# Kernel tuning notes

Hardware: AMD Instinct MI355X
Metric: run time of the kernel (lower is better)

Reference implementation:

```python
import jax, jax.numpy as jnp
import numpy as np

V, E, H, C = 100000, 300, 512, 3
SP, SH, B = 64, 32, 128


def lstm_scan(x, Wih, Whh, b):
    # x: [T, B, E]; PyTorch gate order i, f, g, o
    T, Bb, _ = x.shape
    Hh = Whh.shape[1]
    h0 = jnp.zeros((Bb, Hh), x.dtype)

    def step(carry, xt):
        h, c = carry
        g = xt @ Wih.T + h @ Whh.T + b
        i, f, gg, o = jnp.split(g, 4, axis=-1)
        c = jax.nn.sigmoid(f) * c + jax.nn.sigmoid(i) * jnp.tanh(gg)
        h = jax.nn.sigmoid(o) * jnp.tanh(c)
        return (h, c), h

    _, hs = jax.lax.scan(step, (h0, h0), x)
    return hs  # [T, B, H]


def setup_inputs() -> dict:
    key = jax.random.key(0)
    ks = jax.random.split(key, 20)
    inv_sqrt_h = 1.0 / np.sqrt(H).astype(np.float32)

    def u(k, shape, scale):
        return (jax.random.uniform(k, shape, jnp.float32) * 2.0 - 1.0) * scale

    embed_table = jax.random.normal(ks[4], (V, E), jnp.float32) * 0.1
    embed_table = embed_table.at[0].set(0.0)  # padding_idx=0
    return {
        "premise": jax.random.randint(ks[0], (SP, B), 1, V),
        "premise_len": jax.random.randint(ks[1], (B,), 1, SP + 1),
        "hypothesis": jax.random.randint(ks[2], (SH, B), 1, V),
        "hypothesis_len": jax.random.randint(ks[3], (B,), 1, SH + 1),
        "embed_table": embed_table,
        "p_Wih": u(ks[5], (4 * H, E), inv_sqrt_h),
        "p_Whh": u(ks[6], (4 * H, H), inv_sqrt_h),
        "p_b": u(ks[7], (4 * H,), inv_sqrt_h),
        "h_Wih": u(ks[8], (4 * H, E), inv_sqrt_h),
        "h_Whh": u(ks[9], (4 * H, H), inv_sqrt_h),
        "h_b": u(ks[10], (4 * H,), inv_sqrt_h),
        "m_Wih": u(ks[11], (4 * H, 2 * H), inv_sqrt_h),
        "m_Whh": u(ks[12], (4 * H, H), inv_sqrt_h),
        "m_b": u(ks[13], (4 * H,), inv_sqrt_h),
        "w_e": jax.random.uniform(ks[14], (H,), jnp.float32),
        "Ws": u(ks[15], (H, H), np.sqrt(6.0 / (2 * H)).astype(np.float32)),
        "Wt": u(ks[16], (H, H), np.sqrt(6.0 / (2 * H)).astype(np.float32)),
        "Wm": u(ks[17], (H, H), np.sqrt(6.0 / (2 * H)).astype(np.float32)),
        "fc_W": u(ks[18], (C, H), np.sqrt(6.0 / (H + C)).astype(np.float32)),
        "fc_b": jnp.zeros((C,), jnp.float32),
    }


def reference(premise, premise_len, hypothesis, hypothesis_len, embed_table,
              p_Wih, p_Whh, p_b, h_Wih, h_Whh, h_b, m_Wih, m_Whh, m_b,
              w_e, Ws, Wt, Wm, fc_W, fc_b):
    Sp, Bb = premise.shape
    Sh = hypothesis.shape[0]
    Hh = Ws.shape[0]

    # Encoder LSTMs; emulate pack/pad: outputs past length are zeros
    h_s = lstm_scan(embed_table[premise], p_Wih, p_Whh, p_b)  # [Sp,B,H]
    h_s = h_s * (jnp.arange(Sp)[:, None] < premise_len[None, :]).astype(h_s.dtype)[:, :, None]
    h_t = lstm_scan(embed_table[hypothesis], h_Wih, h_Whh, h_b)  # [Sh,B,H]
    h_t = h_t * (jnp.arange(Sh)[:, None] < hypothesis_len[None, :]).astype(h_t.dtype)[:, :, None]

    Ws_hs = jnp.einsum('sbe,he->sbh', h_s, Ws)  # precompute premise projection

    def step(carry, inputs):
        h_m, c_m, h_last = carry
        h_t_k, k = inputs
        q = h_t_k @ Wt.T + h_m @ Wm.T                              # [B,H]
        e = jnp.einsum('sbh,h->sb', jnp.tanh(Ws_hs + q[None]), w_e)  # [Sp,B]
        alpha = jax.nn.softmax(e, axis=0)                           # softmax over premise (no mask, as in original)
        a_k = jnp.einsum('sb,sbh->bh', alpha, h_s)
        m_k = jnp.concatenate([a_k, h_t_k], axis=1)                 # [B,2H]
        g = m_k @ m_Wih.T + h_m @ m_Whh.T + m_b
        i, f, gg, o = jnp.split(g, 4, axis=-1)
        c_new = jax.nn.sigmoid(f) * c_m + jax.nn.sigmoid(i) * jnp.tanh(gg)
        h_new = jax.nn.sigmoid(o) * jnp.tanh(c_new)
        h_last = jnp.where((k + 1 == hypothesis_len)[:, None], h_new, h_last)
        return (h_new, c_new, h_last), None

    z = jnp.zeros((Bb, Hh), h_s.dtype)
    (_, _, h_last), _ = jax.lax.scan(step, (z, z, z), (h_t, jnp.arange(Sh)))
    return h_last @ fc_W.T + fc_b  # [B, C]
```

## Files before the change

kernel.cpp:

```cpp
#include <hip/hip_runtime.h>


#define NWG 256
#define TPB 512

typedef float f8v __attribute__((ext_vector_type(8)));

#define O_XPP      0ull
#define O_HTMW     0ull
#define O_HTWT     8388608ull
#define O_WSHS     10485760ull
#define O_XPH      16777216ull
#define O_HST      25165824ull
#define O_HS2      29360128ull
#define O_HTT      33554432ull
#define O_WIHTP    35651584ull
#define O_WIHTH    36265984ull
#define O_WHHPP    36880384ull
#define O_WHHPH    37928960ull
#define O_DW       38977536ull
#define O_WST      41074688ull
#define O_WTT      41336832ull
#define O_MWIHRT   41598976ull
#define O_BPP      42647552ull
#define O_BPH      42649600ull
#define O_BPM      42651648ull
#define O_HT2      42653696ull
#define O_HMT2     42784768ull
#define O_QBUF     42915840ull
#define O_AK2      42981376ull
#define O_HLAST    43046912ull
#define WS_FLOATS  43112448ull

__device__ unsigned g_cnt = 0u;
__device__ unsigned g_gen = 0u;
__device__ unsigned g_arr[NWG * 16];
__device__ unsigned g_relA[16 * 16];
__device__ unsigned g_base = 0u;

struct Params {
  const int* premise; const int* plen; const int* hyp; const int* hlen;
  const float* embed;
  const float* pWih; const float* pWhh; const float* pb;
  const float* hWih; const float* hWhh; const float* hb;
  const float* mWih; const float* mWhh; const float* mb;
  const float* we; const float* Ws; const float* Wt; const float* Wm;
  const float* fcW; const float* fcb;
  float* out; float* ws;
};

__device__ __forceinline__ float2 sysld2(const float* p){
  unsigned long long u = __hip_atomic_load((const unsigned long long*)p,
      __ATOMIC_RELAXED, __HIP_MEMORY_SCOPE_SYSTEM);
  union { unsigned long long u; float2 f; } c; c.u = u; return c.f;
}
__device__ __forceinline__ void sysst(float* p, float v){
  union { float f; unsigned u; } c; c.f = v;
  __hip_atomic_store((unsigned*)p, c.u, __ATOMIC_RELAXED, __HIP_MEMORY_SCOPE_SYSTEM);
}

__device__ __forceinline__ void gbarH(){
  __syncthreads();
  if (threadIdx.x == 0){
    __threadfence();
    unsigned snap = __hip_atomic_load(&g_gen, __ATOMIC_RELAXED, __HIP_MEMORY_SCOPE_AGENT);
    unsigned n = __hip_atomic_fetch_add(&g_cnt, 1u, __ATOMIC_ACQ_REL, __HIP_MEMORY_SCOPE_AGENT);
    if ((n & 255u) == 255u){
      __hip_atomic_store(&g_gen, snap + 1u, __ATOMIC_RELEASE, __HIP_MEMORY_SCOPE_AGENT);
    } else {
      unsigned g;
      do {
        __builtin_amdgcn_s_sleep(2);
        g = __hip_atomic_load(&g_gen, __ATOMIC_ACQUIRE, __HIP_MEMORY_SCOPE_AGENT);
      } while ((int)(g - snap) <= 0);
    }
  }
  __syncthreads();
}

__device__ __forceinline__ void gbarL(unsigned e, int wg, int tid){
  __syncthreads();
  if (wg == 0){
    if (tid == 0)
      __hip_atomic_store(&g_arr[0], e, __ATOMIC_RELAXED, __HIP_MEMORY_SCOPE_SYSTEM);
    if (tid < NWG){
      while ((int)(__hip_atomic_load(&g_arr[tid*16], __ATOMIC_RELAXED,
                                     __HIP_MEMORY_SCOPE_SYSTEM) - e) < 0)
        __builtin_amdgcn_s_sleep(1);
    }
    __syncthreads();
    if (tid < 16)
      __hip_atomic_store(&g_relA[tid*16], e, __ATOMIC_RELAXED, __HIP_MEMORY_SCOPE_SYSTEM);
  } else {
    if (tid == 0){
      __hip_atomic_store(&g_arr[wg*16], e, __ATOMIC_RELAXED, __HIP_MEMORY_SCOPE_SYSTEM);
      while ((int)(__hip_atomic_load(&g_relA[(wg & 15)*16], __ATOMIC_RELAXED,
                                     __HIP_MEMORY_SCOPE_SYSTEM) - e) < 0)
        __builtin_amdgcn_s_sleep(1);
    }
    __syncthreads();
  }
}

__device__ __forceinline__ float sigf(float x){ return 1.0f/(1.0f + __expf(-x)); }
__device__ __forceinline__ float tanhf_(float x){ return 2.0f/(1.0f + __expf(-2.0f*x)) - 1.0f; }

__device__ __forceinline__ float wsum(float v){
  #pragma unroll
  for (int o = 32; o > 0; o >>= 1) v += __shfl_xor(v, o, 64);
  return v;
}
__device__ __forceinline__ float wmaxr(float v){
  #pragma unroll
  for (int o = 32; o > 0; o >>= 1) v = fmaxf(v, __shfl_xor(v, o, 64));
  return v;
}

__device__ void lstm_enc(int wg, int tid, int cg, int bg, int T,
    const float* __restrict__ XP, const float* __restrict__ WPair,
    const int* __restrict__ lens, float* hbuf,
    float* __restrict__ houtT, float* __restrict__ hout2, float* lds,
    unsigned& ep)
{
  const int b8 = tid & 7, hc32 = (tid >> 3) & 31, gp = tid >> 8;
  const int b = bg*8 + b8, hc = cg*32 + hc32;
  const float* wrow = WPair + (size_t)(hc*2 + gp) * 1024;
  const int mylen = lens[b];
  const int sb = tid >> 6, sk = (tid & 63) * 8;
  float* stage = lds;
  float* xch   = lds + 8*516;
  float c_reg = 0.f;

  for (int t = 0; t < T; ++t){
    const float* hin  = hbuf + (size_t)(t & 1) * 65536;
    float*       hout = hbuf + (size_t)((t + 1) & 1) * 65536;
    {
      const float* src = hin + (size_t)(bg*8 + sb)*512 + sk;
      float2 v0 = sysld2(src), v1 = sysld2(src+2), v2 = sysld2(src+4), v3 = sysld2(src+6);
      float* dst = stage + sb*516 + sk;
      float4 w0 = {v0.x, v0.y, v1.x, v1.y};
      float4 w1 = {v2.x, v2.y, v3.x, v3.y};
      *(float4*)dst = w0; *(float4*)(dst+4) = w1;
    }
    __syncthreads();
    float a0 = 0.f, a1 = 0.f;
    const float* hr = stage + b8*516;
    #pragma unroll 2
    for (int k = 0; k < 512; k += 4){
      float4 h4 = *(const float4*)(hr + k);
      float4 wA = *(const float4*)(wrow + k*2);
      float4 wB = *(const float4*)(wrow + k*2 + 4);
      a0 += h4.x*wA.x + h4.y*wA.z + h4.z*wB.x + h4.w*wB.z;
      a1 += h4.x*wA.y + h4.y*wA.w + h4.z*wB.y + h4.w*wB.w;
    }
    float2 xg = *(const float2*)(XP + ((size_t)t*128 + b)*2048 + hc*4 + gp*2);
    a0 += xg.x; a1 += xg.y;
    if (gp == 1){ xch[(b8*32+hc32)*2+0] = a0; xch[(b8*32+hc32)*2+1] = a1; }
    __syncthreads();
    if (gp == 0){
      float gg = xch[(b8*32+hc32)*2+0], go = xch[(b8*32+hc32)*2+1];
      float iv = sigf(a0), fv = sigf(a1), gv = tanhf_(gg), ov = sigf(go);
      c_reg = fv * c_reg + iv * gv;
      float hv = ov * tanhf_(c_reg);
      sysst(hout + (size_t)b*512 + hc, hv);
      float hm = (t < mylen) ? hv : 0.f;
      houtT[((size_t)t*512 + hc)*128 + b] = hm;
      if (hout2) hout2[((size_t)t*128 + b)*512 + hc] = hm;
    }
    ++ep; gbarL(ep, wg, tid);
  }
}

__global__ __launch_bounds__(TPB, 2) void mlstm(Params p){
  const int wg = blockIdx.x, tid = threadIdx.x;
  const int lane = tid & 63, wave = tid >> 6;
  const int gtid = wg * TPB + tid;
  const int gwave = wg * 8 + wave;
  const int cg = wg & 15, bg = wg >> 4;
  __shared__ float lds[8736];
  __shared__ unsigned sh_base;

  if (tid == 0)
    sh_base = __hip_atomic_load(&g_base, __ATOMIC_RELAXED, __HIP_MEMORY_SCOPE_SYSTEM);
  __syncthreads();
  unsigned ep = sh_base;

  float* const ws     = p.ws;
  float* const XPp    = ws + O_XPP;
  float* const XPh    = ws + O_XPH;
  float* const htmW   = ws + O_HTMW;
  float* const htWt   = ws + O_HTWT;
  float* const Ws_hs  = ws + O_WSHS;
  float* const h_sT   = ws + O_HST;
  float* const h_s2   = ws + O_HS2;
  float* const h_tT   = ws + O_HTT;
  float* const WihTp  = ws + O_WIHTP;
  float* const WihTh  = ws + O_WIHTH;
  float* const WhhPP  = ws + O_WHHPP;
  float* const WhhPH  = ws + O_WHHPH;
  float* const DW     = ws + O_DW;
  float* const WsT    = ws + O_WST;
  float* const WtT    = ws + O_WTT;
  float* const mWihRT = ws + O_MWIHRT;
  float* const bpP    = ws + O_BPP;
  float* const bpH    = ws + O_BPH;
  float* const bpM    = ws + O_BPM;
  float* const hT2    = ws + O_HT2;
  float* const hmT2   = ws + O_HMT2;
  float* const qbuf   = ws + O_QBUF;
  float* const ak2    = ws + O_AK2;
  float* const hlast  = ws + O_HLAST;

  for (int idx = gtid; idx < 300*2048; idx += NWG*TPB){
    int e = idx >> 11, jp = idx & 2047;
    int oc = (jp & 3) * 512 + (jp >> 2);
    WihTp[idx] = p.pWih[(size_t)oc*300 + e];
    WihTh[idx] = p.hWih[(size_t)oc*300 + e];
  }
  for (int idx = gtid; idx < 1024*512*2; idx += NWG*TPB){
    int g = idx & 1, k = (idx >> 1) & 511, pp = idx >> 10;
    int hc = pp >> 1, gp = pp & 1, oc = (gp*2+g)*512 + hc;
    WhhPP[idx] = p.pWhh[(size_t)oc*512 + k];
    WhhPH[idx] = p.hWhh[(size_t)oc*512 + k];
  }
  for (int idx = gtid; idx < 1024*1024*2; idx += NWG*TPB){
    int g = idx & 1, k = (idx >> 1) & 1023, pp = idx >> 11;
    int hc = pp >> 1, gp = pp & 1, oc = (gp*2+g)*512 + hc;
    DW[idx] = (k < 512) ? p.mWih[(size_t)oc*1024 + k]
                        : p.mWhh[(size_t)oc*512 + (k - 512)];
  }
  for (int idx = gtid; idx < 512*512; idx += NWG*TPB){
    int k = idx >> 9, h = idx & 511;
    WsT[idx] = p.Ws[(size_t)h*512 + k];
    WtT[idx] = p.Wt[(size_t)h*512 + k];
  }
  for (int idx = gtid; idx < 512*2048; idx += NWG*TPB){
    int k = idx >> 11, jp = idx & 2047;
    int oc = (jp & 3) * 512 + (jp >> 2);
    mWihRT[idx] = p.mWih[(size_t)oc*1024 + 512 + k];
  }
  for (int idx = gtid; idx < 2048; idx += NWG*TPB){
    int oc = (idx & 3) * 512 + (idx >> 2);
    bpP[idx] = p.pb[oc]; bpH[idx] = p.hb[oc]; bpM[idx] = p.mb[oc];
  }
  for (int idx = gtid; idx < 131072; idx += NWG*TPB){ hT2[idx] = 0.f; hmT2[idx] = 0.f; }
  gbarH();

  for (int task = gwave; task < 6144; task += NWG*8){
    const bool prem = task < 4096;
    int rb, cb;
    if (prem){ cb = task >> 10; rb = task & 1023; }
    else { int t2 = task - 4096; cb = t2 >> 9; rb = t2 & 511; }
    const int r0 = rb * 8;
    const int* toks = prem ? p.premise : p.hyp;
    const float* wT = prem ? WihTp : WihTh;
    const float* bias = prem ? bpP : bpH;
    float* outp = prem ? XPp : XPh;
    const int j0 = cb * 512 + lane * 8;
    const float* xr[8];
    #pragma unroll
    for (int r = 0; r < 8; ++r) xr[r] = p.embed + (size_t)toks[r0 + r] * 300;
    f8v bias8 = *(const f8v*)(bias + j0);
    float acc[8][8];
    #pragma unroll
    for (int r = 0; r < 8; ++r){
      #pragma unroll
      for (int i = 0; i < 8; ++i) acc[r][i] = 0.f;
    }
    for (int e = 0; e < 300; ++e){
      f8v w8 = *(const f8v*)(wT + (size_t)e * 2048 + j0);
      #pragma unroll
      for (int r = 0; r < 8; ++r){
        float xv = xr[r][e];
        #pragma unroll
        for (int i = 0; i < 8; ++i) acc[r][i] += xv * w8[i];
      }
    }
    #pragma unroll
    for (int r = 0; r < 8; ++r){
      f8v o8;
      #pragma unroll
      for (int i = 0; i < 8; ++i) o8[i] = acc[r][i] + bias8[i];
      *(f8v*)(outp + (size_t)(r0 + r) * 2048 + j0) = o8;
    }
  }
  gbarH();

  lstm_enc(wg, tid, cg, bg, 64, XPp, WhhPP, p.plen, hT2, h_sT, h_s2, lds, ep);
  for (int idx = gtid; idx < 65536; idx += NWG*TPB) sysst(hT2 + idx, 0.f);
  ++ep; gbarL(ep, wg, tid);
  lstm_enc(wg, tid, cg, bg, 32, XPh, WhhPH, p.hlen, hT2, h_tT, nullptr, lds, ep);
  gbarH();

  for (int task = gwave; task < 3584; task += NWG*8){
    const float* src; const float* wT; const float* bias; float* outp;
    int rb, cb, cols;
    if (task < 1024){ rb = task;        cb = 0;            src = h_sT; wT = WsT;    bias = nullptr; outp = Ws_hs; cols = 512; }
    else if (task < 1536){ rb = task-1024; cb = 0;         src = h_tT; wT = WtT;    bias = nullptr; outp = htWt;  cols = 512; }
    else { int t2 = task - 1536; cb = t2 >> 9; rb = t2 & 511; src = h_tT; wT = mWihRT; bias = bpM;  outp = htmW;  cols = 2048; }
    const int r0 = rb * 8;
    const int j0 = cb * 512 + lane * 8;
    const float* xr[8];
    #pragma unroll
    for (int r = 0; r < 8; ++r){
      int row = r0 + r;
      xr[r] = src + (size_t)(row >> 7) * 65536 + (row & 127);
    }
    f8v bias8 = {0,0,0,0,0,0,0,0};
    if (bias) bias8 = *(const f8v*)(bias + j0);
    float acc[8][8];
    #pragma unroll
    for (int r = 0; r < 8; ++r){
      #pragma unroll
      for (int i = 0; i < 8; ++i) acc[r][i] = 0.f;
    }
    for (int k = 0; k < 512; ++k){
      f8v w8 = *(const f8v*)(wT + (size_t)k * cols + j0);
      #pragma unroll
      for (int r = 0; r < 8; ++r){
        float xv = xr[r][(size_t)k * 128];
        #pragma unroll
        for (int i = 0; i < 8; ++i) acc[r][i] += xv * w8[i];
      }
    }
    #pragma unroll
    for (int r = 0; r < 8; ++r){
      f8v o8;
      #pragma unroll
      for (int i = 0; i < 8; ++i) o8[i] = acc[r][i] + bias8[i];
      *(f8v*)(outp + (size_t)(r0 + r) * (size_t)cols + j0) = o8;
    }
  }
  gbarH();

  const int b8 = tid & 7, hc32 = (tid >> 3) & 31, gp = tid >> 8;
  const int mb_ = bg*8 + b8, mhc = cg*32 + hc32;
  const float* dwrow = DW + (size_t)(mhc*2 + gp) * 2048;
  const int hyplen_b = p.hlen[mb_];
  const int sb = tid >> 6, sk = (tid & 63) * 8;
  float* stage  = lds;
  float* xchA   = lds + 8*516;
  float* stage2 = lds;
  float* xch2   = lds + 8*1028;
  float cm_reg = 0.f, hl_reg = 0.f;

  for (int k = 0; k < 32; ++k){
    const float* hmin  = hmT2 + (size_t)(k & 1) * 65536;
    float*       hmout = hmT2 + (size_t)((k + 1) & 1) * 65536;

    {
      {
        const float* src = hmin + (size_t)(bg*8 + sb)*512 + sk;
        float2 v0 = sysld2(src), v1 = sysld2(src+2), v2 = sysld2(src+4), v3 = sysld2(src+6);
        float* dst = stage + sb*516 + sk;
        float4 w0 = {v0.x, v0.y, v1.x, v1.y};
        float4 w1 = {v2.x, v2.y, v3.x, v3.y};
        *(float4*)dst = w0; *(float4*)(dst+4) = w1;
      }
      __syncthreads();
      const int c32 = (tid >> 3) & 31, half = tid >> 8;
      const int c = cg*32 + c32;
      float a = 0.f;
      const float* hr = stage + b8*516 + half*256;
      const float* wr = p.Wm + (size_t)c*512 + half*256;
      #pragma unroll 2
      for (int kk = 0; kk < 256; kk += 4){
        float4 h4 = *(const float4*)(hr + kk);
        float4 w4 = *(const float4*)(wr + kk);
        a += h4.x*w4.x + h4.y*w4.y + h4.z*w4.z + h4.w*w4.w;
      }
      if (half == 1) xchA[c32*8 + b8] = a;
      __syncthreads();
      if (half == 0){
        float v = a + xchA[c32*8 + b8] + htWt[((size_t)k*128 + mb_)*512 + c];
        sysst(qbuf + (size_t)mb_*512 + c, v);
      }
    }
    ++ep; gbarL(ep, wg, tid);

    if (wg < 128){
      const int bb = wg;
      const float* qb = qbuf + (size_t)bb*512 + lane*8;
      float2 qa = sysld2(qb), qbv = sysld2(qb+2), qc = sysld2(qb+4), qd = sysld2(qb+6);
      float4 q0 = {qa.x, qa.y, qbv.x, qbv.y};
      float4 q1 = {qc.x, qc.y, qd.x, qd.y};
      float4 e0 = *(const float4*)(p.we + lane*8);
      float4 e1 = *(const float4*)(p.we + lane*8 + 4);
      #pragma unroll
      for (int si = 0; si < 8; ++si){
        int s = wave*8 + si;
        const float* wsr = Ws_hs + ((size_t)s*128 + bb)*512 + lane*8;
        float4 s0 = *(const float4*)wsr;
        float4 s1 = *(const float4*)(wsr + 4);
        float v = tanhf_(s0.x + q0.x)*e0.x + tanhf_(s0.y + q0.y)*e0.y
                + tanhf_(s0.z + q0.z)*e0.z + tanhf_(s0.w + q0.w)*e0.w
                + tanhf_(s1.x + q1.x)*e1.x + tanhf_(s1.y + q1.y)*e1.y
                + tanhf_(s1.z + q1.z)*e1.z + tanhf_(s1.w + q1.w)*e1.w;
        v = wsum(v);
        if (lane == 0) lds[s] = v;
      }
      __syncthreads();
      if (wave == 0){
        float v = lds[lane];
        float m = wmaxr(v);
        float ex = __expf(v - m);
        float sm = wsum(ex);
        lds[64 + lane] = ex / sm;
      }
      __syncthreads();
      {
        float acc = 0.f;
        const float* hsb = h_s2 + (size_t)bb*512 + tid;
        #pragma unroll 4
        for (int s = 0; s < 64; s += 4){
          float4 al = *(const float4*)(lds + 64 + s);
          acc += al.x * hsb[(size_t)(s+0)*65536]
               + al.y * hsb[(size_t)(s+1)*65536]
               + al.z * hsb[(size_t)(s+2)*65536]
               + al.w * hsb[(size_t)(s+3)*65536];
        }
        sysst(ak2 + (size_t)bb*512 + tid, acc);
      }
    }
    ++ep; gbarL(ep, wg, tid);

    {
      {
        const int sb2 = tid >> 6, c0 = (tid & 63) * 16;
        const float* src = (c0 < 512) ? (ak2 + (size_t)(bg*8 + sb2)*512 + c0)
                                      : (hmin + (size_t)(bg*8 + sb2)*512 + (c0 - 512));
        float* dst = stage2 + sb2*1028 + c0;
        #pragma unroll
        for (int i = 0; i < 16; i += 4){
          float2 va = sysld2(src + i), vb = sysld2(src + i + 2);
          float4 w = {va.x, va.y, vb.x, vb.y};
          *(float4*)(dst + i) = w;
        }
      }
      __syncthreads();
      float a0 = 0.f, a1 = 0.f;
      const float* hr = stage2 + b8*1028;
      #pragma unroll 2
      for (int kk = 0; kk < 1024; kk += 4){
        float4 h4 = *(const float4*)(hr + kk);
        float4 wA = *(const float4*)(dwrow + kk*2);
        float4 wB = *(const float4*)(dwrow + kk*2 + 4);
        a0 += h4.x*wA.x + h4.y*wA.z + h4.z*wB.x + h4.w*wB.z;
        a1 += h4.x*wA.y + h4.y*wA.w + h4.z*wB.y + h4.w*wB.w;
      }
      float2 xg = *(const float2*)(htmW + ((size_t)k*128 + mb_)*2048 + mhc*4 + gp*2);
      a0 += xg.x; a1 += xg.y;
      if (gp == 1){ xch2[(b8*32+hc32)*2+0] = a0; xch2[(b8*32+hc32)*2+1] = a1; }
      __syncthreads();
      if (gp == 0){
        float gg = xch2[(b8*32+hc32)*2+0], go = xch2[(b8*32+hc32)*2+1];
        float iv = sigf(a0), fv = sigf(a1), gv = tanhf_(gg), ov = sigf(go);
        cm_reg = fv * cm_reg + iv * gv;
        float hv = ov * tanhf_(cm_reg);
        sysst(hmout + (size_t)mb_*512 + mhc, hv);
        if (k + 1 == hyplen_b) hl_reg = hv;
      }
    }
    ++ep; gbarL(ep, wg, tid);
  }

  if (gp == 0) hlast[(size_t)mb_*512 + mhc] = hl_reg;
  gbarH();

  if (wg == 0 && tid == 0)
    __hip_atomic_store(&g_base, ep, __ATOMIC_RELAXED, __HIP_MEMORY_SCOPE_SYSTEM);

  if (wg == 0){
    for (int o = wave; o < 384; o += 8){
      int bb = o / 3, cls = o - bb*3;
      const float* hr = hlast + (size_t)bb*512 + lane*8;
      const float* wr = p.fcW + (size_t)cls*512 + lane*8;
      float4 h0 = *(const float4*)hr, h1 = *(const float4*)(hr + 4);
      float4 w0 = *(const float4*)wr, w1 = *(const float4*)(wr + 4);
      float v = h0.x*w0.x + h0.y*w0.y + h0.z*w0.z + h0.w*w0.w
              + h1.x*w1.x + h1.y*w1.y + h1.z*w1.z + h1.w*w1.w;
      v = wsum(v);
      if (lane == 0) p.out[o] = v + p.fcb[cls];
    }
  }
}

extern "C" void kernel_launch(void* const* d_in, const int* in_sizes, int n_in,
                              void* d_out, int out_size, void* d_ws, size_t ws_size,
                              hipStream_t stream) {
  if (ws_size < WS_FLOATS * sizeof(float)) return;
  Params prm;
  prm.premise = (const int*)d_in[0];
  prm.plen    = (const int*)d_in[1];
  prm.hyp     = (const int*)d_in[2];
  prm.hlen    = (const int*)d_in[3];
  prm.embed   = (const float*)d_in[4];
  prm.pWih    = (const float*)d_in[5];
  prm.pWhh    = (const float*)d_in[6];
  prm.pb      = (const float*)d_in[7];
  prm.hWih    = (const float*)d_in[8];
  prm.hWhh    = (const float*)d_in[9];
  prm.hb      = (const float*)d_in[10];
  prm.mWih    = (const float*)d_in[11];
  prm.mWhh    = (const float*)d_in[12];
  prm.mb      = (const float*)d_in[13];
  prm.we      = (const float*)d_in[14];
  prm.Ws      = (const float*)d_in[15];
  prm.Wt      = (const float*)d_in[16];
  prm.Wm      = (const float*)d_in[17];
  prm.fcW     = (const float*)d_in[18];
  prm.fcb     = (const float*)d_in[19];
  prm.out     = (float*)d_out;
  prm.ws      = (float*)d_ws;
  mlstm<<<dim3(NWG), dim3(TPB), 0, stream>>>(prm);
}
```

Baseline: 4.635 ms.

## Replace global barriers with per-group dataflow flags in recurrent LSTM loops

Replaces the all-workgroup gbarL barrier between recurrent steps with per-workgroup epoch flags, so each workgroup waits only on the 16 peer workgroups (or attention rows) whose outputs it actually consumes. The step-zero hidden-state loads and matvecs are skipped, which removes the need to zero the ping-pong buffers and the barrier between encoders. This cuts global synchronization latency on the serial critical path. It adds fragile epoch bookkeeping across kernel launches, with base values persisted in global flags.

New measurement: 4.465 ms. -3.7%, faster.

```diff
diff --git a/kernel.cpp b/kernel.cpp
--- a/kernel.cpp
+++ b/kernel.cpp
@@ -34,9 +34,11 @@
 
 __device__ unsigned g_cnt = 0u;
 __device__ unsigned g_gen = 0u;
-__device__ unsigned g_arr[NWG * 16];
-__device__ unsigned g_relA[16 * 16];
-__device__ unsigned g_base = 0u;
+__device__ unsigned g_FE[NWG * 16];
+__device__ unsigned g_FA[NWG * 16];
+__device__ unsigned g_FB[NWG * 16];
+__device__ unsigned g_FD[NWG * 16];
+__device__ unsigned g_base2 = 0u;
 
 struct Params {
   const int* premise; const int* plen; const int* hyp; const int* hlen;
@@ -57,6 +59,14 @@
 __device__ __forceinline__ void sysst(float* p, float v){
   union { float f; unsigned u; } c; c.f = v;
   __hip_atomic_store((unsigned*)p, c.u, __ATOMIC_RELAXED, __HIP_MEMORY_SCOPE_SYSTEM);
+}
+__device__ __forceinline__ void fbump(unsigned* a, unsigned v){
+  __hip_atomic_store(a, v, __ATOMIC_RELAXED, __HIP_MEMORY_SCOPE_SYSTEM);
+}
+__device__ __forceinline__ void waitflag(const unsigned* a, unsigned tgt){
+  while ((int)(__hip_atomic_load(a, __ATOMIC_RELAXED,
+               __HIP_MEMORY_SCOPE_SYSTEM) - tgt) < 0)
+    __builtin_amdgcn_s_sleep(1);
 }
 
 __device__ __forceinline__ void gbarH(){
@@ -78,30 +88,6 @@
   __syncthreads();
 }
 
-__device__ __forceinline__ void gbarL(unsigned e, int wg, int tid){
-  __syncthreads();
-  if (wg == 0){
-    if (tid == 0)
-      __hip_atomic_store(&g_arr[0], e, __ATOMIC_RELAXED, __HIP_MEMORY_SCOPE_SYSTEM);
-    if (tid < NWG){
-      while ((int)(__hip_atomic_load(&g_arr[tid*16], __ATOMIC_RELAXED,
-                                     __HIP_MEMORY_SCOPE_SYSTEM) - e) < 0)
-        __builtin_amdgcn_s_sleep(1);
-    }
-    __syncthreads();
-    if (tid < 16)
-      __hip_atomic_store(&g_relA[tid*16], e, __ATOMIC_RELAXED, __HIP_MEMORY_SCOPE_SYSTEM);
-  } else {
-    if (tid == 0){
-      __hip_atomic_store(&g_arr[wg*16], e, __ATOMIC_RELAXED, __HIP_MEMORY_SCOPE_SYSTEM);
-      while ((int)(__hip_atomic_load(&g_relA[(wg & 15)*16], __ATOMIC_RELAXED,
-                                     __HIP_MEMORY_SCOPE_SYSTEM) - e) < 0)
-        __builtin_amdgcn_s_sleep(1);
-    }
-    __syncthreads();
-  }
-}
-
 __device__ __forceinline__ float sigf(float x){ return 1.0f/(1.0f + __expf(-x)); }
 __device__ __forceinline__ float tanhf_(float x){ return 2.0f/(1.0f + __expf(-2.0f*x)) - 1.0f; }
 
@@ -116,11 +102,11 @@
   return v;
 }
 
-__device__ void lstm_enc(int wg, int tid, int cg, int bg, int T,
+__device__ void lstm_enc(int wg, int tid, int lane, int cg, int bg, int T,
     const float* __restrict__ XP, const float* __restrict__ WPair,
     const int* __restrict__ lens, float* hbuf,
     float* __restrict__ houtT, float* __restrict__ hout2, float* lds,
-    unsigned& ep)
+    unsigned tb)
 {
   const int b8 = tid & 7, hc32 = (tid >> 3) & 31, gp = tid >> 8;
   const int b = bg*8 + b8, hc = cg*32 + hc32;
@@ -130,11 +116,13 @@
   float* stage = lds;
   float* xch   = lds + 8*516;
   float c_reg = 0.f;
+  const unsigned* peer = &g_FE[(((unsigned)bg << 4) | (lane & 15)) * 16];
 
   for (int t = 0; t < T; ++t){
     const float* hin  = hbuf + (size_t)(t & 1) * 65536;
     float*       hout = hbuf + (size_t)((t + 1) & 1) * 65536;
-    {
+    if (lane < 16) waitflag(peer, tb + t);
+    if (t > 0){
       const float* src = hin + (size_t)(bg*8 + sb)*512 + sk;
       float2 v0 = sysld2(src), v1 = sysld2(src+2), v2 = sysld2(src+4), v3 = sysld2(src+6);
       float* dst = stage + sb*516 + sk;
@@ -144,14 +132,16 @@
     }
     __syncthreads();
     float a0 = 0.f, a1 = 0.f;
-    const float* hr = stage + b8*516;
-    #pragma unroll 2
-    for (int k = 0; k < 512; k += 4){
-      float4 h4 = *(const float4*)(hr + k);
-      float4 wA = *(const float4*)(wrow + k*2);
-      float4 wB = *(const float4*)(wrow + k*2 + 4);
-      a0 += h4.x*wA.x + h4.y*wA.z + h4.z*wB.x + h4.w*wB.z;
-      a1 += h4.x*wA.y + h4.y*wA.w + h4.z*wB.y + h4.w*wB.w;
+    if (t > 0){
+      const float* hr = stage + b8*516;
+      #pragma unroll 2
+      for (int k = 0; k < 512; k += 4){
+        float4 h4 = *(const float4*)(hr + k);
+        float4 wA = *(const float4*)(wrow + k*2);
+        float4 wB = *(const float4*)(wrow + k*2 + 4);
+        a0 += h4.x*wA.x + h4.y*wA.z + h4.z*wB.x + h4.w*wB.z;
+        a1 += h4.x*wA.y + h4.y*wA.w + h4.z*wB.y + h4.w*wB.w;
+      }
     }
     float2 xg = *(const float2*)(XP + ((size_t)t*128 + b)*2048 + hc*4 + gp*2);
     a0 += xg.x; a1 += xg.y;
@@ -167,7 +157,8 @@
       houtT[((size_t)t*512 + hc)*128 + b] = hm;
       if (hout2) hout2[((size_t)t*128 + b)*512 + hc] = hm;
     }
-    ++ep; gbarL(ep, wg, tid);
+    __syncthreads();
+    if (tid == 0) fbump(&g_FE[wg*16], tb + t + 1);
   }
 }
 
@@ -181,9 +172,9 @@
   __shared__ unsigned sh_base;
 
   if (tid == 0)
-    sh_base = __hip_atomic_load(&g_base, __ATOMIC_RELAXED, __HIP_MEMORY_SCOPE_SYSTEM);
+    sh_base = __hip_atomic_load(&g_base2, __ATOMIC_RELAXED, __HIP_MEMORY_SCOPE_SYSTEM);
   __syncthreads();
-  unsigned ep = sh_base;
+  const unsigned B = sh_base;
 
   float* const ws     = p.ws;
   float* const XPp    = ws + O_XPP;
@@ -243,7 +234,6 @@
     int oc = (idx & 3) * 512 + (idx >> 2);
     bpP[idx] = p.pb[oc]; bpH[idx] = p.hb[oc]; bpM[idx] = p.mb[oc];
   }
-  for (int idx = gtid; idx < 131072; idx += NWG*TPB){ hT2[idx] = 0.f; hmT2[idx] = 0.f; }
   gbarH();
 
   for (int task = gwave; task < 6144; task += NWG*8){
@@ -286,10 +276,8 @@
   }
   gbarH();
 
-  lstm_enc(wg, tid, cg, bg, 64, XPp, WhhPP, p.plen, hT2, h_sT, h_s2, lds, ep);
-  for (int idx = gtid; idx < 65536; idx += NWG*TPB) sysst(hT2 + idx, 0.f);
-  ++ep; gbarL(ep, wg, tid);
-  lstm_enc(wg, tid, cg, bg, 32, XPh, WhhPH, p.hlen, hT2, h_tT, nullptr, lds, ep);
+  lstm_enc(wg, tid, lane, cg, bg, 64, XPp, WhhPP, p.plen, hT2, h_sT, h_s2, lds, B);
+  lstm_enc(wg, tid, lane, cg, bg, 32, XPh, WhhPH, p.hlen, hT2, h_tT, nullptr, lds, B + 64);
   gbarH();
 
   for (int task = gwave; task < 3584; task += NWG*8){
@@ -343,31 +331,37 @@
   float* stage2 = lds;
   float* xch2   = lds + 8*1028;
   float cm_reg = 0.f, hl_reg = 0.f;
+  const unsigned* peerFD = &g_FD[(((unsigned)bg << 4) | (lane & 15)) * 16];
+  const unsigned* rowFB  = &g_FB[((unsigned)(bg*8) + (lane & 7)) * 16];
 
   for (int k = 0; k < 32; ++k){
     const float* hmin  = hmT2 + (size_t)(k & 1) * 65536;
     float*       hmout = hmT2 + (size_t)((k + 1) & 1) * 65536;
 
+    if (lane < 16) waitflag(peerFD, B + k);
+    else if (lane < 24) waitflag(&g_FB[((unsigned)(bg*8) + (lane - 16)) * 16], B + k);
+    if (k > 0){
+      const float* src = hmin + (size_t)(bg*8 + sb)*512 + sk;
+      float2 v0 = sysld2(src), v1 = sysld2(src+2), v2 = sysld2(src+4), v3 = sysld2(src+6);
+      float* dst = stage + sb*516 + sk;
+      float4 w0 = {v0.x, v0.y, v1.x, v1.y};
+      float4 w1 = {v2.x, v2.y, v3.x, v3.y};
+      *(float4*)dst = w0; *(float4*)(dst+4) = w1;
+    }
+    __syncthreads();
     {
-      {
-        const float* src = hmin + (size_t)(bg*8 + sb)*512 + sk;
-        float2 v0 = sysld2(src), v1 = sysld2(src+2), v2 = sysld2(src+4), v3 = sysld2(src+6);
-        float* dst = stage + sb*516 + sk;
-        float4 w0 = {v0.x, v0.y, v1.x, v1.y};
-        float4 w1 = {v2.x, v2.y, v3.x, v3.y};
-        *(float4*)dst = w0; *(float4*)(dst+4) = w1;
-      }
-      __syncthreads();
       const int c32 = (tid >> 3) & 31, half = tid >> 8;
       const int c = cg*32 + c32;
       float a = 0.f;
-      const float* hr = stage + b8*516 + half*256;
-      const float* wr = p.Wm + (size_t)c*512 + half*256;
-      #pragma unroll 2
-      for (int kk = 0; kk < 256; kk += 4){
-        float4 h4 = *(const float4*)(hr + kk);
-        float4 w4 = *(const float4*)(wr + kk);
-        a += h4.x*w4.x + h4.y*w4.y + h4.z*w4.z + h4.w*w4.w;
+      if (k > 0){
+        const float* hr = stage + b8*516 + half*256;
+        const float* wr = p.Wm + (size_t)c*512 + half*256;
+        #pragma unroll 2
+        for (int kk = 0; kk < 256; kk += 4){
+          float4 h4 = *(const float4*)(hr + kk);
+          float4 w4 = *(const float4*)(wr + kk);
+          a += h4.x*w4.x + h4.y*w4.y + h4.z*w4.z + h4.w*w4.w;
+        }
       }
       if (half == 1) xchA[c32*8 + b8] = a;
       __syncthreads();
@@ -376,10 +370,13 @@
         sysst(qbuf + (size_t)mb_*512 + c, v);
       }
     }
-    ++ep; gbarL(ep, wg, tid);
+    __syncthreads();
+    if (tid == 0) fbump(&g_FA[wg*16], B + k + 1);
 
     if (wg < 128){
       const int bb = wg;
+      if (lane < 16) waitflag(&g_FA[(((unsigned)(bb >> 3) << 4) | lane) * 16], B + k + 1);
+      else if (lane < 32) waitflag(&g_FD[(((unsigned)(bb >> 3) << 4) | (lane - 16)) * 16], B + k);
       const float* qb = qbuf + (size_t)bb*512 + lane*8;
       float2 qa = sysld2(qb), qbv = sysld2(qb+2), qc = sysld2(qb+4), qd = sysld2(qb+6);
       float4 q0 = {qa.x, qa.y, qbv.x, qbv.y};
@@ -421,23 +418,38 @@
         }
         sysst(ak2 + (size_t)bb*512 + tid, acc);
       }
-    }
-    ++ep; gbarL(ep, wg, tid);
-
+      __syncthreads();
+      if (tid == 0) fbump(&g_FB[wg*16], B + k + 1);
+    }
+
+    if (lane < 8) waitflag(rowFB, B + k + 1);
     {
-      {
-        const int sb2 = tid >> 6, c0 = (tid & 63) * 16;
-        const float* src = (c0 < 512) ? (ak2 + (size_t)(bg*8 + sb2)*512 + c0)
-                                      : (hmin + (size_t)(bg*8 + sb2)*512 + (c0 - 512));
-        float* dst = stage2 + sb2*1028 + c0;
+      const int sb2 = tid >> 6, c0 = (tid & 63) * 16;
+      float* dst = stage2 + sb2*1028 + c0;
+      if (c0 < 512){
+        const float* src = ak2 + (size_t)(bg*8 + sb2)*512 + c0;
         #pragma unroll
         for (int i = 0; i < 16; i += 4){
           float2 va = sysld2(src + i), vb = sysld2(src + i + 2);
           float4 w = {va.x, va.y, vb.x, vb.y};
           *(float4*)(dst + i) = w;
         }
-      }
-      __syncthreads();
+      } else if (k > 0){
+        const float* src = hmin + (size_t)(bg*8 + sb2)*512 + (c0 - 512);
+        #pragma unroll
+        for (int i = 0; i < 16; i += 4){
+          float2 va = sysld2(src + i), vb = sysld2(src + i + 2);
+          float4 w = {va.x, va.y, vb.x, vb.y};
+          *(float4*)(dst + i) = w;
+        }
+      } else {
+        float4 z = {0.f, 0.f, 0.f, 0.f};
+        #pragma unroll
+        for (int i = 0; i < 16; i += 4) *(float4*)(dst + i) = z;
+      }
+    }
+    __syncthreads();
+    {
       float a0 = 0.f, a1 = 0.f;
       const float* hr = stage2 + b8*1028;
       #pragma unroll 2
@@ -461,14 +473,21 @@
         if (k + 1 == hyplen_b) hl_reg = hv;
       }
     }
-    ++ep; gbarL(ep, wg, tid);
+    __syncthreads();
+    if (tid == 0) fbump(&g_FD[wg*16], B + k + 1);
   }
 
   if (gp == 0) hlast[(size_t)mb_*512 + mhc] = hl_reg;
   gbarH();
 
-  if (wg == 0 && tid == 0)
-    __hip_atomic_store(&g_base, ep, __ATOMIC_RELAXED, __HIP_MEMORY_SCOPE_SYSTEM);
+  if (tid == 0){
+    fbump(&g_FE[wg*16], B + 4096);
+    fbump(&g_FA[wg*16], B + 4096);
+    fbump(&g_FB[wg*16], B + 4096);
+    fbump(&g_FD[wg*16], B + 4096);
+    if (wg == 0)
+      __hip_atomic_store(&g_base2, B + 4096, __ATOMIC_RELAXED, __HIP_MEMORY_SCOPE_SYSTEM);
+  }
 
   if (wg == 0){
     for (int o = wave; o < 384; o += 8){
```
